# Kernel optimization log

Hardware: AMD Instinct MI355X
Metric: run time of the kernel (lower is better)

The kernel has to match this reference:

```python
import jax, jax.numpy as jnp
import numpy as np

N_ATOMS = 50000
N_PAIRS = 600000
F = 128          # number_of_per_atom_features
RBF = 16         # number_of_radial_basis_functions
N_INT_RES = 3    # interaction residual blocks
N_OUT_RES = 2    # output residual blocks
N_PROPS = 2      # atomic properties (hardcoded in PhysNetModule)


def setup_inputs() -> dict:
    key = jax.random.key(0)
    ks = jax.random.split(key, 24)
    s = 1.0 / np.sqrt(F)
    inp = {
        "atomic_embedding": jax.random.normal(ks[0], (N_ATOMS, F), jnp.float32),
        "f_ij": jax.random.uniform(ks[1], (N_PAIRS, RBF), jnp.float32),
        "pair_indices": jax.random.randint(ks[2], (2, N_PAIRS), 0, N_ATOMS, jnp.int64),
        # attention_mask: Dense(RBF -> F, bias=False); zero-init in source, randomized here
        "Wg": jax.random.normal(ks[3], (RBF, F), jnp.float32) * (1.0 / np.sqrt(RBF)),
        "Wi": jax.random.normal(ks[4], (F, F), jnp.float32) * s,
        "bi": jnp.zeros((F,), jnp.float32),
        "Wj": jax.random.normal(ks[5], (F, F), jnp.float32) * s,
        "bj": jnp.zeros((F,), jnp.float32),
        "Wv": jax.random.normal(ks[6], (F, F), jnp.float32) * s,
        "bv": jnp.zeros((F,), jnp.float32),
        "gate": jnp.ones((F,), jnp.float32),
        "int_res_W1": jax.random.normal(ks[7], (N_INT_RES, F, F), jnp.float32) * s,
        "int_res_b1": jnp.zeros((N_INT_RES, F), jnp.float32),
        "int_res_W2": jax.random.normal(ks[8], (N_INT_RES, F, F), jnp.float32) * s,
        "int_res_b2": jnp.zeros((N_INT_RES, F), jnp.float32),
        "out_res_W1": jax.random.normal(ks[9], (N_OUT_RES, F, F), jnp.float32) * s,
        "out_res_b1": jnp.zeros((N_OUT_RES, F), jnp.float32),
        "out_res_W2": jax.random.normal(ks[10], (N_OUT_RES, F, F), jnp.float32) * s,
        "out_res_b2": jnp.zeros((N_OUT_RES, F), jnp.float32),
        # output head: Dense(F -> 2), zero-init in source, randomized here
        "Wo": jax.random.normal(ks[11], (F, N_PROPS), jnp.float32) * s,
        "bo": jnp.zeros((N_PROPS,), jnp.float32),
    }
    return inp


def _residual(x, W1, b1, W2, b2):
    # PhysNetResidual: x + Dense(Dense(act(x), act), linear)
    h = jax.nn.softplus(x)
    h = jax.nn.softplus(h @ W1 + b1)
    return x + h @ W2 + b2


def reference(atomic_embedding, f_ij, pair_indices,
              Wg, Wi, bi, Wj, bj, Wv, bv, gate,
              int_res_W1, int_res_b1, int_res_W2, int_res_b2,
              out_res_W1, out_res_b1, out_res_W2, out_res_b2,
              Wo, bo):
    idx_i, idx_j = pair_indices[0], pair_indices[1]

    # --- interaction module ---
    e = jax.nn.softplus(atomic_embedding)            # [N, F]
    g = f_ij @ Wg                                    # [E, F] attention mask (no bias)
    u = jax.nn.softplus(e @ Wi + bi)                 # [N, F] interaction_i
    m_j = jax.nn.softplus(e[idx_j] @ Wj + bj) * g    # [E, F] gather + gate
    u = u.at[idx_i].add(m_j)                         # scatter_add to i-atoms
    for k in range(N_INT_RES):
        u = _residual(u, int_res_W1[k], int_res_b1[k], int_res_W2[k], int_res_b2[k])
    u = jax.nn.softplus(u)
    v = gate * e + (u @ Wv + bv)                     # updated embedding [N, F]

    # --- output module ---
    x = v
    for k in range(N_OUT_RES):
        x = _residual(x, out_res_W1[k], out_res_b1[k], out_res_W2[k], out_res_b2[k])
    prediction = x @ Wo + bo                         # [N, 2]
    return prediction, v
```

## Files before the change

### kernel.cpp

```cpp
#include <hip/hip_runtime.h>
#include <math.h>

#define F 128
#define RBF 16
#define NATOMS 50000
#define NPAIRS 600000
#define NBLK 196

typedef float f32x4 __attribute__((ext_vector_type(4)));
typedef short s16x8 __attribute__((ext_vector_type(8)));

__device__ __forceinline__ float sp(float x) {
    return fmaxf(x, 0.f) + __logf(1.f + __expf(-fabsf(x)));
}
__device__ __forceinline__ unsigned short f2bf(float x) {
    unsigned u = __float_as_uint(x);
    u += 0x7FFFu + ((u >> 16) & 1u);
    return (unsigned short)(u >> 16);
}
__device__ __forceinline__ float bf2f(unsigned short u) {
    return __uint_as_float(((unsigned)u) << 16);
}

__global__ __launch_bounds__(256) void prep_w_k(
    const float* __restrict__ Wi, const float* __restrict__ Wj, const float* __restrict__ Wv,
    const float* __restrict__ iW1, const float* __restrict__ iW2,
    const float* __restrict__ oW1, const float* __restrict__ oW2,
    short* __restrict__ wpack)
{
    int o = blockIdx.x * 256 + threadIdx.x;
    if (o >= 13 * 16384) return;
    int mat = o >> 14;
    int rem = o & 16383;
    int j = rem & 7;
    int lane = (rem >> 3) & 63;
    int nt = (rem >> 9) & 7;
    int kc = rem >> 12;
    int k = kc * 32 + ((lane >> 4) << 3) + j;
    int n = nt * 16 + (lane & 15);
    const float* src;
    if (mat == 0) src = Wi;
    else if (mat == 1) src = Wj;
    else if (mat == 2) src = Wv;
    else if (mat < 6) src = iW1 + (size_t)(mat - 3) * 16384;
    else if (mat < 9) src = iW2 + (size_t)(mat - 6) * 16384;
    else if (mat < 11) src = oW1 + (size_t)(mat - 9) * 16384;
    else src = oW2 + (size_t)(mat - 11) * 16384;
    wpack[o] = (short)f2bf(src[(size_t)k * F + n]);
}

template <int PRE>
__device__ __forceinline__ s16x8 load_a_frag(const float* __restrict__ in,
                                             int row, int nrows, int kc, int cg)
{
    s16x8 a;
    if (row < nrows) {
        const float* p = in + (size_t)row * F + kc * 32 + cg * 8;
        float4 x0 = *(const float4*)p;
        float4 x1 = *(const float4*)(p + 4);
        if (PRE) {
            x0.x = sp(x0.x); x0.y = sp(x0.y); x0.z = sp(x0.z); x0.w = sp(x0.w);
            x1.x = sp(x1.x); x1.y = sp(x1.y); x1.z = sp(x1.z); x1.w = sp(x1.w);
        }
        a[0] = f2bf(x0.x); a[1] = f2bf(x0.y); a[2] = f2bf(x0.z); a[3] = f2bf(x0.w);
        a[4] = f2bf(x1.x); a[5] = f2bf(x1.y); a[6] = f2bf(x1.z); a[7] = f2bf(x1.w);
    } else {
#pragma unroll
        for (int i = 0; i < 8; ++i) a[i] = 0;
    }
    return a;
}

template <int PRE, int POST, int DUAL>
__global__ __launch_bounds__(256) void mgemm_k(
    const float* __restrict__ in, const short* __restrict__ wpA,
    const float* __restrict__ bA, float* __restrict__ outA,
    const short* __restrict__ wpB, const float* __restrict__ bB,
    unsigned short* __restrict__ outB, int nrows)
{
    const int lane = threadIdx.x & 63;
    const int wv = threadIdx.x >> 6;
    const int grp = wv >> 1, half = wv & 1;
    const int r0 = blockIdx.x * 32 + grp * 16;
    const int cl = lane & 15, cg = lane >> 4;
    const int ntb = half * 4;

    s16x8 afr[4];
#pragma unroll
    for (int kc = 0; kc < 4; ++kc) afr[kc] = load_a_frag<PRE>(in, r0 + cl, nrows, kc, cg);

    f32x4 accA[4], accB[4];
#pragma unroll
    for (int n = 0; n < 4; ++n) {
        accA[n] = (f32x4){0.f, 0.f, 0.f, 0.f};
        accB[n] = (f32x4){0.f, 0.f, 0.f, 0.f};
    }

#pragma unroll
    for (int kc = 0; kc < 4; ++kc) {
        const s16x8* bpA = (const s16x8*)wpA + (size_t)(kc * 8 + ntb) * 64 + lane;
#pragma unroll
        for (int n = 0; n < 4; ++n) {
            s16x8 b = bpA[n * 64];
            accA[n] = __builtin_amdgcn_mfma_f32_16x16x32_bf16(afr[kc], b, accA[n], 0, 0, 0);
        }
        if (DUAL) {
            const s16x8* bpB = (const s16x8*)wpB + (size_t)(kc * 8 + ntb) * 64 + lane;
#pragma unroll
            for (int n = 0; n < 4; ++n) {
                s16x8 b = bpB[n * 64];
                accB[n] = __builtin_amdgcn_mfma_f32_16x16x32_bf16(afr[kc], b, accB[n], 0, 0, 0);
            }
        }
    }

#pragma unroll
    for (int n = 0; n < 4; ++n) {
        const int col = (ntb + n) * 16 + cl;
        const float ba = bA[col];
        const float bb = DUAL ? bB[col] : 0.f;
#pragma unroll
        for (int q = 0; q < 4; ++q) {
            const int row = r0 + cg * 4 + q;
            if (row < nrows) {
                const size_t o = (size_t)row * F + col;
                float val = accA[n][q] + ba;
                if (POST == 1) val = sp(val);
                outA[o] = val;
                if (DUAL) outB[o] = f2bf(sp(accB[n][q] + bb));
            }
        }
    }
}

__device__ __forceinline__ void gemm_half(const short* __restrict__ wp, int lane, int ntb,
                                          const s16x8 afr[4], f32x4 acc[4])
{
#pragma unroll
    for (int n = 0; n < 4; ++n) acc[n] = (f32x4){0.f, 0.f, 0.f, 0.f};
#pragma unroll
    for (int kc = 0; kc < 4; ++kc) {
        const s16x8* bp = (const s16x8*)wp + (size_t)(kc * 8 + ntb) * 64 + lane;
#pragma unroll
        for (int n = 0; n < 4; ++n) {
            s16x8 b = bp[n * 64];
            acc[n] = __builtin_amdgcn_mfma_f32_16x16x32_bf16(afr[kc], b, acc[n], 0, 0, 0);
        }
    }
}

template <int FIRST>
__device__ __forceinline__ void residual_half(
    const float* __restrict__ u, f32x4 xreg[4],
    unsigned short* __restrict__ S, unsigned short* __restrict__ H,
    const short* __restrict__ wp1, const float* __restrict__ b1,
    const short* __restrict__ wp2, const float* __restrict__ b2,
    int r0, int nrows, int lane, int cl, int cg, int ntb)
{
    s16x8 afr[4];
    if (FIRST) {
#pragma unroll
        for (int kc = 0; kc < 4; ++kc) afr[kc] = load_a_frag<1>(u, r0 + cl, nrows, kc, cg);
    } else {
#pragma unroll
        for (int kc = 0; kc < 4; ++kc)
            afr[kc] = *(const s16x8*)(S + cl * 144 + kc * 32 + cg * 8);
    }
    f32x4 acc[4];
    gemm_half(wp1, lane, ntb, afr, acc);
#pragma unroll
    for (int n = 0; n < 4; ++n) {
        const int col = (ntb + n) * 16 + cl;
        const float bb = b1[col];
#pragma unroll
        for (int q = 0; q < 4; ++q)
            H[(cg * 4 + q) * 144 + col] = f2bf(sp(acc[n][q] + bb));
    }
    __syncthreads();
#pragma unroll
    for (int kc = 0; kc < 4; ++kc)
        afr[kc] = *(const s16x8*)(H + cl * 144 + kc * 32 + cg * 8);
    gemm_half(wp2, lane, ntb, afr, acc);
#pragma unroll
    for (int n = 0; n < 4; ++n) {
        const int col = (ntb + n) * 16 + cl;
        const float bb = b2[col];
#pragma unroll
        for (int q = 0; q < 4; ++q) {
            float xv = xreg[n][q] + acc[n][q] + bb;
            xreg[n][q] = xv;
            S[(cg * 4 + q) * 144 + col] = f2bf(sp(xv));
        }
    }
    __syncthreads();
}

__global__ __launch_bounds__(128, 6) void fused_tail_k(
    const float* __restrict__ u, const float* __restrict__ emb,
    const float* __restrict__ gate,
    const short* __restrict__ wpI1, const float* __restrict__ ib1,
    const short* __restrict__ wpI2, const float* __restrict__ ib2,
    const short* __restrict__ wpWv, const float* __restrict__ bvv,
    const short* __restrict__ wpO1, const float* __restrict__ ob1,
    const short* __restrict__ wpO2, const float* __restrict__ ob2,
    const float* __restrict__ Wo, const float* __restrict__ bo,
    float* __restrict__ vout, float* __restrict__ pred, int nrows)
{
    __shared__ unsigned short S[16 * 144];
    __shared__ unsigned short H[16 * 144];
    const int lane = threadIdx.x & 63;
    const int half = threadIdx.x >> 6;
    const int r0 = blockIdx.x * 16;
    const int cl = lane & 15, cg = lane >> 4;
    const int ntb = half * 4;

    f32x4 xreg[4];
#pragma unroll
    for (int n = 0; n < 4; ++n) {
        const int col = (ntb + n) * 16 + cl;
#pragma unroll
        for (int q = 0; q < 4; ++q) {
            const int row = r0 + cg * 4 + q;
            xreg[n][q] = (row < nrows) ? u[(size_t)row * F + col] : 0.f;
        }
    }

    residual_half<1>(u, xreg, S, H, wpI1, ib1, wpI2, ib2,
                     r0, nrows, lane, cl, cg, ntb);
    for (int k = 1; k < 3; ++k)
        residual_half<0>(u, xreg, S, H,
                         wpI1 + (size_t)k * 16384, ib1 + (size_t)k * F,
                         wpI2 + (size_t)k * 16384, ib2 + (size_t)k * F,
                         r0, nrows, lane, cl, cg, ntb);

    {
        s16x8 afr[4];
#pragma unroll
        for (int kc = 0; kc < 4; ++kc)
            afr[kc] = *(const s16x8*)(S + cl * 144 + kc * 32 + cg * 8);
        f32x4 acc[4];
        gemm_half(wpWv, lane, ntb, afr, acc);
        __syncthreads();
#pragma unroll
        for (int n = 0; n < 4; ++n) {
            const int col = (ntb + n) * 16 + cl;
            const float bb = bvv[col];
            const float gt = gate[col];
#pragma unroll
            for (int q = 0; q < 4; ++q) {
                const int row = r0 + cg * 4 + q;
                float val = acc[n][q] + bb;
                if (row < nrows) {
                    const size_t o = (size_t)row * F + col;
                    val += gt * sp(emb[o]);
                    vout[o] = val;
                }
                xreg[n][q] = val;
                S[(cg * 4 + q) * 144 + col] = f2bf(sp(val));
            }
        }
        __syncthreads();
    }

    for (int k = 0; k < 2; ++k)
        residual_half<0>(u, xreg, S, H,
                         wpO1 + (size_t)k * 16384, ob1 + (size_t)k * F,
                         wpO2 + (size_t)k * 16384, ob2 + (size_t)k * F,
                         r0, nrows, lane, cl, cg, ntb);

    {
        float2 wo[4];
#pragma unroll
        for (int n = 0; n < 4; ++n)
            wo[n] = *(const float2*)(Wo + (size_t)((ntb + n) * 16 + cl) * 2);
        float* sc = (float*)S;
#pragma unroll
        for (int q = 0; q < 4; ++q) {
            float a0 = xreg[0][q] * wo[0].x + xreg[1][q] * wo[1].x
                     + xreg[2][q] * wo[2].x + xreg[3][q] * wo[3].x;
            float a1 = xreg[0][q] * wo[0].y + xreg[1][q] * wo[1].y
                     + xreg[2][q] * wo[2].y + xreg[3][q] * wo[3].y;
#pragma unroll
            for (int m = 1; m < 16; m <<= 1) {
                a0 += __shfl_xor(a0, m);
                a1 += __shfl_xor(a1, m);
            }
            if (cl == 0) {
                sc[half * 32 + (cg * 4 + q) * 2 + 0] = a0;
                sc[half * 32 + (cg * 4 + q) * 2 + 1] = a1;
            }
        }
        __syncthreads();
        if (half == 0 && lane < 16) {
            const int row = r0 + lane;
            if (row < nrows) {
                pred[(size_t)row * 2 + 0] = sc[lane * 2 + 0] + sc[32 + lane * 2 + 0] + bo[0];
                pred[(size_t)row * 2 + 1] = sc[lane * 2 + 1] + sc[32 + lane * 2 + 1] + bo[1];
            }
        }
    }
}

__global__ void hist_k(const int* __restrict__ idx_i, int* __restrict__ counts)
{
    int p = blockIdx.x * blockDim.x + threadIdx.x;
    if (p < NPAIRS) atomicAdd(&counts[idx_i[p]], 1);
}

__global__ __launch_bounds__(256) void scan1_k(
    const int* __restrict__ counts, int* __restrict__ bsum)
{
    __shared__ int red[256];
    const int t = threadIdx.x;
    const int i = blockIdx.x * 256 + t;
    red[t] = (i < NATOMS) ? counts[i] : 0;
    __syncthreads();
#pragma unroll
    for (int s = 128; s > 0; s >>= 1) {
        if (t < s) red[t] += red[t + s];
        __syncthreads();
    }
    if (t == 0) bsum[blockIdx.x] = red[0];
}

__global__ __launch_bounds__(256) void scan2_k(
    const int* __restrict__ bsum, int* __restrict__ bbase, int* __restrict__ offsets)
{
    __shared__ int sh[256];
    const int t = threadIdx.x;
    const int v = (t < NBLK) ? bsum[t] : 0;
    sh[t] = v;
    __syncthreads();
#pragma unroll
    for (int s = 1; s < 256; s <<= 1) {
        int add = (t >= s) ? sh[t - s] : 0;
        __syncthreads();
        sh[t] += add;
        __syncthreads();
    }
    if (t < NBLK) bbase[t] = sh[t] - v;
    if (t == 0) offsets[NATOMS] = NPAIRS;
}

__global__ __launch_bounds__(256) void scan3_k(
    const int* __restrict__ counts, const int* __restrict__ bbase,
    int* __restrict__ offsets, int* __restrict__ cursor)
{
    __shared__ int sh[256];
    const int t = threadIdx.x;
    const int i = blockIdx.x * 256 + t;
    const int v = (i < NATOMS) ? counts[i] : 0;
    sh[t] = v;
    __syncthreads();
#pragma unroll
    for (int s = 1; s < 256; s <<= 1) {
        int add = (t >= s) ? sh[t - s] : 0;
        __syncthreads();
        sh[t] += add;
        __syncthreads();
    }
    if (i < NATOMS) {
        const int off = bbase[blockIdx.x] + sh[t] - v;
        offsets[i] = off;
        cursor[i] = off;
    }
}

__global__ void scatter_k(const int* __restrict__ idx_i, const int* __restrict__ idx_j,
                          int* __restrict__ cursor, int2* __restrict__ jplist)
{
    int p = blockIdx.x * blockDim.x + threadIdx.x;
    if (p < NPAIRS) {
        int pos = atomicAdd(&cursor[idx_i[p]], 1);
        jplist[pos] = make_int2(idx_j[p], p);
    }
}

__device__ __forceinline__ void gpair(const float* __restrict__ fp,
                                      const float* wg0, const float* wg1,
                                      float& g0, float& g1)
{
    float4 A = ((const float4*)fp)[0], B = ((const float4*)fp)[1];
    float4 C = ((const float4*)fp)[2], D = ((const float4*)fp)[3];
    g0 = A.x*wg0[0] + A.y*wg0[1] + A.z*wg0[2] + A.w*wg0[3]
       + B.x*wg0[4] + B.y*wg0[5] + B.z*wg0[6] + B.w*wg0[7]
       + C.x*wg0[8] + C.y*wg0[9] + C.z*wg0[10] + C.w*wg0[11]
       + D.x*wg0[12] + D.y*wg0[13] + D.z*wg0[14] + D.w*wg0[15];
    g1 = A.x*wg1[0] + A.y*wg1[1] + A.z*wg1[2] + A.w*wg1[3]
       + B.x*wg1[4] + B.y*wg1[5] + B.z*wg1[6] + B.w*wg1[7]
       + C.x*wg1[8] + C.y*wg1[9] + C.z*wg1[10] + C.w*wg1[11]
       + D.x*wg1[12] + D.y*wg1[13] + D.z*wg1[14] + D.w*wg1[15];
}

__global__ __launch_bounds__(256) void gather_k(
    const unsigned short* __restrict__ mj, const float* __restrict__ fij,
    const int2* __restrict__ jplist, const int* __restrict__ offsets,
    const float* __restrict__ Wg, float* __restrict__ u)
{
    const int lane = threadIdx.x & 63;
    const int atom = blockIdx.x * 4 + (threadIdx.x >> 6);
    const int f0 = lane * 2;

    float wg0[16], wg1[16];
#pragma unroll
    for (int r = 0; r < 16; ++r) {
        float2 w = *(const float2*)(Wg + r * F + f0);
        wg0[r] = w.x; wg1[r] = w.y;
    }

    const int k0 = offsets[atom], k1 = offsets[atom + 1];
    float acc0 = 0.f, acc1 = 0.f;

    for (int k = k0; k < k1; k += 16) {
        int2 jp[16];
#pragma unroll
        for (int t = 0; t < 16; ++t) {
            const int kk = (k + t < k1) ? (k + t) : (k1 - 1);
            jp[t] = jplist[kk];
        }
        unsigned m[16];
        const float* fp[16];
#pragma unroll
        for (int t = 0; t < 16; ++t) {
            const int js = __builtin_amdgcn_readfirstlane(jp[t].x);
            const int ps = __builtin_amdgcn_readfirstlane(jp[t].y);
            m[t] = *(const unsigned*)(mj + (size_t)js * F + f0);
            fp[t] = fij + (size_t)ps * RBF;
        }
#pragma unroll
        for (int t = 0; t < 16; ++t) {
            float g0, g1;
            gpair(fp[t], wg0, wg1, g0, g1);
            if (k + t >= k1) { g0 = 0.f; g1 = 0.f; }
            acc0 += bf2f((unsigned short)(m[t] & 0xFFFF)) * g0;
            acc1 += bf2f((unsigned short)(m[t] >> 16))    * g1;
        }
    }

    float2* up = (float2*)(u + (size_t)atom * F + f0);
    float2 old = *up;
    old.x += acc0; old.y += acc1;
    *up = old;
}

extern "C" void kernel_launch(void* const* d_in, const int* in_sizes, int n_in,
                              void* d_out, int out_size, void* d_ws, size_t ws_size,
                              hipStream_t stream)
{
    const float* emb   = (const float*)d_in[0];
    const float* fij   = (const float*)d_in[1];
    const int*   pidx  = (const int*)d_in[2];
    const float* Wg    = (const float*)d_in[3];
    const float* Wi    = (const float*)d_in[4];
    const float* bi    = (const float*)d_in[5];
    const float* Wj    = (const float*)d_in[6];
    const float* bj    = (const float*)d_in[7];
    const float* Wv    = (const float*)d_in[8];
    const float* bv    = (const float*)d_in[9];
    const float* gate  = (const float*)d_in[10];
    const float* iW1   = (const float*)d_in[11];
    const float* ib1   = (const float*)d_in[12];
    const float* iW2   = (const float*)d_in[13];
    const float* ib2   = (const float*)d_in[14];
    const float* oW1   = (const float*)d_in[15];
    const float* ob1   = (const float*)d_in[16];
    const float* oW2   = (const float*)d_in[17];
    const float* ob2   = (const float*)d_in[18];
    const float* Wo    = (const float*)d_in[19];
    const float* bo    = (const float*)d_in[20];

    const int* idx_i = pidx;
    const int* idx_j = pidx + NPAIRS;

    float* outp = (float*)d_out;
    float* pred = outp;
    float* v    = outp + (size_t)NATOMS * 2;

    const size_t NF = (size_t)NATOMS * F;
    float* u = (float*)d_ws;
    unsigned short* mj = (unsigned short*)(u + NF);
    short* wpack = (short*)(mj + NF);
    int* counts   = (int*)(wpack + 13 * 16384);
    int* offsets  = counts + NATOMS;
    int* cursor   = offsets + NATOMS + 1;
    int2* jplist  = (int2*)(cursor + NATOMS);
    int* bsum     = (int*)(jplist + NPAIRS);
    int* bbase    = bsum + NBLK;

    const short* wpWi = wpack;
    const short* wpWj = wpack + 1 * 16384;
    const short* wpWv = wpack + 2 * 16384;
    const short* wpI1 = wpack + 3 * 16384;
    const short* wpI2 = wpack + 6 * 16384;
    const short* wpO1 = wpack + 9 * 16384;
    const short* wpO2 = wpack + 11 * 16384;

    prep_w_k<<<(13 * 16384 + 255) / 256, 256, 0, stream>>>(Wi, Wj, Wv, iW1, iW2, oW1, oW2, wpack);
    hipMemsetAsync(counts, 0, NATOMS * sizeof(int), stream);
    hist_k<<<(NPAIRS + 255) / 256, 256, 0, stream>>>(idx_i, counts);
    scan1_k<<<NBLK, 256, 0, stream>>>(counts, bsum);
    scan2_k<<<1, 256, 0, stream>>>(bsum, bbase, offsets);
    scan3_k<<<NBLK, 256, 0, stream>>>(counts, bbase, offsets, cursor);
    scatter_k<<<(NPAIRS + 255) / 256, 256, 0, stream>>>(idx_i, idx_j, cursor, jplist);

    mgemm_k<1, 1, 1><<<(NATOMS + 31) / 32, 256, 0, stream>>>(
        emb, wpWi, bi, u, wpWj, bj, mj, NATOMS);

    gather_k<<<(NATOMS + 3) / 4, 256, 0, stream>>>(
        mj, fij, jplist, offsets, Wg, u);

    fused_tail_k<<<(NATOMS + 15) / 16, 128, 0, stream>>>(
        u, emb, gate,
        wpI1, ib1, wpI2, ib2,
        wpWv, bv,
        wpO1, ob1, wpO2, ob2,
        Wo, bo, v, pred, NATOMS);
}
```

Measured before the change: 289.9 us.

## Process two 16-row tiles per wave in fused tail to reuse weight fragments

Each wave in the fused residual-tail kernel now computes two 16-row tiles (A and B) at once. Every weight fragment loaded from global memory feeds two MFMAs instead of one, which halves weight-load traffic per row and gives the MFMA unit independent work to interleave. Blocks grow to 256 threads covering 64 rows, with doubled shared buffers per group. The cost is roughly double the accumulator and register state per thread, which may cut occupancy (launch bounds drop to 4 blocks per CU) or cause spills.

Result: slower. 329.5 us (+13.7%).

```diff
diff --git a/kernel.cpp b/kernel.cpp
--- a/kernel.cpp
+++ b/kernel.cpp
@@ -133,69 +133,94 @@
     }
 }
 
-__device__ __forceinline__ void gemm_half(const short* __restrict__ wp, int lane, int ntb,
-                                          const s16x8 afr[4], f32x4 acc[4])
-{
-#pragma unroll
-    for (int n = 0; n < 4; ++n) acc[n] = (f32x4){0.f, 0.f, 0.f, 0.f};
+template <int FIRST>
+__device__ __forceinline__ void residual_dual(
+    const float* __restrict__ u, f32x4 xA[4], f32x4 xB[4],
+    unsigned short* __restrict__ SA, unsigned short* __restrict__ HA,
+    unsigned short* __restrict__ SB, unsigned short* __restrict__ HB,
+    const short* __restrict__ wp1, const float* __restrict__ b1,
+    const short* __restrict__ wp2, const float* __restrict__ b2,
+    int r0A, int r0B, int nrows, int lane, int cl, int cg, int ntb)
+{
+    s16x8 aA[4], aB[4];
+    if (FIRST) {
+#pragma unroll
+        for (int kc = 0; kc < 4; ++kc) {
+            aA[kc] = load_a_frag<1>(u, r0A + cl, nrows, kc, cg);
+            aB[kc] = load_a_frag<1>(u, r0B + cl, nrows, kc, cg);
+        }
+    } else {
+#pragma unroll
+        for (int kc = 0; kc < 4; ++kc) {
+            aA[kc] = *(const s16x8*)(SA + cl * 144 + kc * 32 + cg * 8);
+            aB[kc] = *(const s16x8*)(SB + cl * 144 + kc * 32 + cg * 8);
+        }
+    }
+    f32x4 cA[4], cB[4];
+#pragma unroll
+    for (int n = 0; n < 4; ++n) {
+        cA[n] = (f32x4){0.f, 0.f, 0.f, 0.f};
+        cB[n] = (f32x4){0.f, 0.f, 0.f, 0.f};
+    }
 #pragma unroll
     for (int kc = 0; kc < 4; ++kc) {
-        const s16x8* bp = (const s16x8*)wp + (size_t)(kc * 8 + ntb) * 64 + lane;
+        const s16x8* bp = (const s16x8*)wp1 + (size_t)(kc * 8 + ntb) * 64 + lane;
 #pragma unroll
         for (int n = 0; n < 4; ++n) {
             s16x8 b = bp[n * 64];
-            acc[n] = __builtin_amdgcn_mfma_f32_16x16x32_bf16(afr[kc], b, acc[n], 0, 0, 0);
-        }
-    }
-}
-
-template <int FIRST>
-__device__ __forceinline__ void residual_half(
-    const float* __restrict__ u, f32x4 xreg[4],
-    unsigned short* __restrict__ S, unsigned short* __restrict__ H,
-    const short* __restrict__ wp1, const float* __restrict__ b1,
-    const short* __restrict__ wp2, const float* __restrict__ b2,
-    int r0, int nrows, int lane, int cl, int cg, int ntb)
-{
-    s16x8 afr[4];
-    if (FIRST) {
-#pragma unroll
-        for (int kc = 0; kc < 4; ++kc) afr[kc] = load_a_frag<1>(u, r0 + cl, nrows, kc, cg);
-    } else {
-#pragma unroll
-        for (int kc = 0; kc < 4; ++kc)
-            afr[kc] = *(const s16x8*)(S + cl * 144 + kc * 32 + cg * 8);
-    }
-    f32x4 acc[4];
-    gemm_half(wp1, lane, ntb, afr, acc);
+            cA[n] = __builtin_amdgcn_mfma_f32_16x16x32_bf16(aA[kc], b, cA[n], 0, 0, 0);
+            cB[n] = __builtin_amdgcn_mfma_f32_16x16x32_bf16(aB[kc], b, cB[n], 0, 0, 0);
+        }
+    }
 #pragma unroll
     for (int n = 0; n < 4; ++n) {
         const int col = (ntb + n) * 16 + cl;
         const float bb = b1[col];
 #pragma unroll
-        for (int q = 0; q < 4; ++q)
-            H[(cg * 4 + q) * 144 + col] = f2bf(sp(acc[n][q] + bb));
+        for (int q = 0; q < 4; ++q) {
+            HA[(cg * 4 + q) * 144 + col] = f2bf(sp(cA[n][q] + bb));
+            HB[(cg * 4 + q) * 144 + col] = f2bf(sp(cB[n][q] + bb));
+        }
     }
     __syncthreads();
 #pragma unroll
-    for (int kc = 0; kc < 4; ++kc)
-        afr[kc] = *(const s16x8*)(H + cl * 144 + kc * 32 + cg * 8);
-    gemm_half(wp2, lane, ntb, afr, acc);
+    for (int kc = 0; kc < 4; ++kc) {
+        aA[kc] = *(const s16x8*)(HA + cl * 144 + kc * 32 + cg * 8);
+        aB[kc] = *(const s16x8*)(HB + cl * 144 + kc * 32 + cg * 8);
+    }
+#pragma unroll
+    for (int n = 0; n < 4; ++n) {
+        cA[n] = (f32x4){0.f, 0.f, 0.f, 0.f};
+        cB[n] = (f32x4){0.f, 0.f, 0.f, 0.f};
+    }
+#pragma unroll
+    for (int kc = 0; kc < 4; ++kc) {
+        const s16x8* bp = (const s16x8*)wp2 + (size_t)(kc * 8 + ntb) * 64 + lane;
+#pragma unroll
+        for (int n = 0; n < 4; ++n) {
+            s16x8 b = bp[n * 64];
+            cA[n] = __builtin_amdgcn_mfma_f32_16x16x32_bf16(aA[kc], b, cA[n], 0, 0, 0);
+            cB[n] = __builtin_amdgcn_mfma_f32_16x16x32_bf16(aB[kc], b, cB[n], 0, 0, 0);
+        }
+    }
 #pragma unroll
     for (int n = 0; n < 4; ++n) {
         const int col = (ntb + n) * 16 + cl;
         const float bb = b2[col];
 #pragma unroll
         for (int q = 0; q < 4; ++q) {
-            float xv = xreg[n][q] + acc[n][q] + bb;
-            xreg[n][q] = xv;
-            S[(cg * 4 + q) * 144 + col] = f2bf(sp(xv));
+            float xa = xA[n][q] + cA[n][q] + bb;
+            float xb = xB[n][q] + cB[n][q] + bb;
+            xA[n][q] = xa;
+            xB[n][q] = xb;
+            SA[(cg * 4 + q) * 144 + col] = f2bf(sp(xa));
+            SB[(cg * 4 + q) * 144 + col] = f2bf(sp(xb));
         }
     }
     __syncthreads();
 }
 
-__global__ __launch_bounds__(128, 6) void fused_tail_k(
+__global__ __launch_bounds__(256, 4) void fused_tail_k(
     const float* __restrict__ u, const float* __restrict__ emb,
     const float* __restrict__ gate,
     const short* __restrict__ wpI1, const float* __restrict__ ib1,
@@ -206,40 +231,66 @@
     const float* __restrict__ Wo, const float* __restrict__ bo,
     float* __restrict__ vout, float* __restrict__ pred, int nrows)
 {
-    __shared__ unsigned short S[16 * 144];
-    __shared__ unsigned short H[16 * 144];
+    __shared__ unsigned short SAb[2][16 * 144];
+    __shared__ unsigned short HAb[2][16 * 144];
+    __shared__ unsigned short SBb[2][16 * 144];
+    __shared__ unsigned short HBb[2][16 * 144];
     const int lane = threadIdx.x & 63;
-    const int half = threadIdx.x >> 6;
-    const int r0 = blockIdx.x * 16;
+    const int wv = threadIdx.x >> 6;
+    const int grp = wv >> 1, half = wv & 1;
+    const int r0A = blockIdx.x * 64 + grp * 32;
+    const int r0B = r0A + 16;
     const int cl = lane & 15, cg = lane >> 4;
     const int ntb = half * 4;
-
-    f32x4 xreg[4];
+    unsigned short* SA = SAb[grp];
+    unsigned short* HA = HAb[grp];
+    unsigned short* SB = SBb[grp];
+    unsigned short* HB = HBb[grp];
+
+    f32x4 xA[4], xB[4];
 #pragma unroll
     for (int n = 0; n < 4; ++n) {
         const int col = (ntb + n) * 16 + cl;
 #pragma unroll
         for (int q = 0; q < 4; ++q) {
-            const int row = r0 + cg * 4 + q;
-            xreg[n][q] = (row < nrows) ? u[(size_t)row * F + col] : 0.f;
-        }
-    }
-
-    residual_half<1>(u, xreg, S, H, wpI1, ib1, wpI2, ib2,
-                     r0, nrows, lane, cl, cg, ntb);
+            const int rA = r0A + cg * 4 + q;
+            const int rB = r0B + cg * 4 + q;
+            xA[n][q] = (rA < nrows) ? u[(size_t)rA * F + col] : 0.f;
+            xB[n][q] = (rB < nrows) ? u[(size_t)rB * F + col] : 0.f;
+        }
+    }
+
+    residual_dual<1>(u, xA, xB, SA, HA, SB, HB, wpI1, ib1, wpI2, ib2,
+                     r0A, r0B, nrows, lane, cl, cg, ntb);
     for (int k = 1; k < 3; ++k)
-        residual_half<0>(u, xreg, S, H,
+        residual_dual<0>(u, xA, xB, SA, HA, SB, HB,
                          wpI1 + (size_t)k * 16384, ib1 + (size_t)k * F,
                          wpI2 + (size_t)k * 16384, ib2 + (size_t)k * F,
-                         r0, nrows, lane, cl, cg, ntb);
+                         r0A, r0B, nrows, lane, cl, cg, ntb);
 
     {
-        s16x8 afr[4];
-#pragma unroll
-        for (int kc = 0; kc < 4; ++kc)
-            afr[kc] = *(const s16x8*)(S + cl * 144 + kc * 32 + cg * 8);
-        f32x4 acc[4];
-        gemm_half(wpWv, lane, ntb, afr, acc);
+        s16x8 aA[4], aB[4];
+#pragma unroll
+        for (int kc = 0; kc < 4; ++kc) {
+            aA[kc] = *(const s16x8*)(SA + cl * 144 + kc * 32 + cg * 8);
+            aB[kc] = *(const s16x8*)(SB + cl * 144 + kc * 32 + cg * 8);
+        }
+        f32x4 cA[4], cB[4];
+#pragma unroll
+        for (int n = 0; n < 4; ++n) {
+            cA[n] = (f32x4){0.f, 0.f, 0.f, 0.f};
+            cB[n] = (f32x4){0.f, 0.f, 0.f, 0.f};
+        }
+#pragma unroll
+        for (int kc = 0; kc < 4; ++kc) {
+            const s16x8* bp = (const s16x8*)wpWv + (size_t)(kc * 8 + ntb) * 64 + lane;
+#pragma unroll
+            for (int n = 0; n < 4; ++n) {
+                s16x8 b = bp[n * 64];
+                cA[n] = __builtin_amdgcn_mfma_f32_16x16x32_bf16(aA[kc], b, cA[n], 0, 0, 0);
+                cB[n] = __builtin_amdgcn_mfma_f32_16x16x32_bf16(aB[kc], b, cB[n], 0, 0, 0);
+            }
+        }
         __syncthreads();
 #pragma unroll
         for (int n = 0; n < 4; ++n) {
@@ -248,54 +299,77 @@
             const float gt = gate[col];
 #pragma unroll
             for (int q = 0; q < 4; ++q) {
-                const int row = r0 + cg * 4 + q;
-                float val = acc[n][q] + bb;
-                if (row < nrows) {
-                    const size_t o = (size_t)row * F + col;
-                    val += gt * sp(emb[o]);
-                    vout[o] = val;
+                const int rA = r0A + cg * 4 + q;
+                const int rB = r0B + cg * 4 + q;
+                float va = cA[n][q] + bb;
+                float vb = cB[n][q] + bb;
+                if (rA < nrows) {
+                    const size_t o = (size_t)rA * F + col;
+                    va += gt * sp(emb[o]);
+                    vout[o] = va;
                 }
-                xreg[n][q] = val;
-                S[(cg * 4 + q) * 144 + col] = f2bf(sp(val));
+                if (rB < nrows) {
+                    const size_t o = (size_t)rB * F + col;
+                    vb += gt * sp(emb[o]);
+                    vout[o] = vb;
+                }
+                xA[n][q] = va;
+                xB[n][q] = vb;
+                SA[(cg * 4 + q) * 144 + col] = f2bf(sp(va));
+                SB[(cg * 4 + q) * 144 + col] = f2bf(sp(vb));
             }
         }
         __syncthreads();
     }
 
     for (int k = 0; k < 2; ++k)
-        residual_half<0>(u, xreg, S, H,
+        residual_dual<0>(u, xA, xB, SA, HA, SB, HB,
                          wpO1 + (size_t)k * 16384, ob1 + (size_t)k * F,
                          wpO2 + (size_t)k * 16384, ob2 + (size_t)k * F,
-                         r0, nrows, lane, cl, cg, ntb);
+                         r0A, r0B, nrows, lane, cl, cg, ntb);
 
     {
         float2 wo[4];
 #pragma unroll
         for (int n = 0; n < 4; ++n)
             wo[n] = *(const float2*)(Wo + (size_t)((ntb + n) * 16 + cl) * 2);
-        float* sc = (float*)S;
+        float* scA = (float*)SA;
+        float* scB = (float*)SB;
 #pragma unroll
         for (int q = 0; q < 4; ++q) {
-            float a0 = xreg[0][q] * wo[0].x + xreg[1][q] * wo[1].x
-                     + xreg[2][q] * wo[2].x + xreg[3][q] * wo[3].x;
-            float a1 = xreg[0][q] * wo[0].y + xreg[1][q] * wo[1].y
-                     + xreg[2][q] * wo[2].y + xreg[3][q] * wo[3].y;
+            float a0 = xA[0][q] * wo[0].x + xA[1][q] * wo[1].x
+                     + xA[2][q] * wo[2].x + xA[3][q] * wo[3].x;
+            float a1 = xA[0][q] * wo[0].y + xA[1][q] * wo[1].y
+                     + xA[2][q] * wo[2].y + xA[3][q] * wo[3].y;
+            float b0 = xB[0][q] * wo[0].x + xB[1][q] * wo[1].x
+                     + xB[2][q] * wo[2].x + xB[3][q] * wo[3].x;
+            float b1 = xB[0][q] * wo[0].y + xB[1][q] * wo[1].y
+                     + xB[2][q] * wo[2].y + xB[3][q] * wo[3].y;
 #pragma unroll
             for (int m = 1; m < 16; m <<= 1) {
                 a0 += __shfl_xor(a0, m);
                 a1 += __shfl_xor(a1, m);
+                b0 += __shfl_xor(b0, m);
+                b1 += __shfl_xor(b1, m);
             }
             if (cl == 0) {
-                sc[half * 32 + (cg * 4 + q) * 2 + 0] = a0;
-                sc[half * 32 + (cg * 4 + q) * 2 + 1] = a1;
+                scA[half * 32 + (cg * 4 + q) * 2 + 0] = a0;
+                scA[half * 32 + (cg * 4 + q) * 2 + 1] = a1;
+                scB[half * 32 + (cg * 4 + q) * 2 + 0] = b0;
+                scB[half * 32 + (cg * 4 + q) * 2 + 1] = b1;
             }
         }
         __syncthreads();
         if (half == 0 && lane < 16) {
-            const int row = r0 + lane;
-            if (row < nrows) {
-                pred[(size_t)row * 2 + 0] = sc[lane * 2 + 0] + sc[32 + lane * 2 + 0] + bo[0];
-                pred[(size_t)row * 2 + 1] = sc[lane * 2 + 1] + sc[32 + lane * 2 + 1] + bo[1];
+            const int rA = r0A + lane;
+            const int rB = r0B + lane;
+            if (rA < nrows) {
+                pred[(size_t)rA * 2 + 0] = scA[lane * 2 + 0] + scA[32 + lane * 2 + 0] + bo[0];
+                pred[(size_t)rA * 2 + 1] = scA[lane * 2 + 1] + scA[32 + lane * 2 + 1] + bo[1];
+            }
+            if (rB < nrows) {
+                pred[(size_t)rB * 2 + 0] = scB[lane * 2 + 0] + scB[32 + lane * 2 + 0] + bo[0];
+                pred[(size_t)rB * 2 + 1] = scB[lane * 2 + 1] + scB[32 + lane * 2 + 1] + bo[1];
             }
         }
     }
@@ -509,7 +583,7 @@
     gather_k<<<(NATOMS + 3) / 4, 256, 0, stream>>>(
         mj, fij, jplist, offsets, Wg, u);
 
-    fused_tail_k<<<(NATOMS + 15) / 16, 128, 0, stream>>>(
+    fused_tail_k<<<(NATOMS + 63) / 64, 256, 0, stream>>>(
         u, emb, gate,
         wpI1, ib1, wpI2, ib2,
         wpWv, bv,
```
